# Performance work log

Measured on AMD Instinct MI355X. Metric: run time of the kernel, lower is better.

## Reference

```python
import jax, jax.numpy as jnp
import numpy as np

NUM_ANCHORS = 2
NUM_CLASSES = 20
H = 7
W = 7
IMG_H = 448
IMG_W = 448
NMS_THRESH = 0.7
SCORE_THRESH = 0.05
NBOX = H * W * NUM_ANCHORS  # 98 candidate boxes per image


def _format_outputs(x):
    # x: [b, H*W*(num_anchors*5 + num_classes)] -> decoded boxes/objectness/scores
    b = x.shape[0]
    x = x.reshape(b, H, W, NUM_ANCHORS * 5 + NUM_CLASSES)
    # class scores shared across anchors of a cell (repeat_interleave in torch)
    b_scores = jnp.broadcast_to(
        x[..., -NUM_CLASSES:].reshape(b, H * W, 1, NUM_CLASSES),
        (b, H * W, NUM_ANCHORS, NUM_CLASSES),
    )
    xa = x[..., : NUM_ANCHORS * 5].reshape(b, H, W, NUM_ANCHORS, 5)
    c_x = jnp.arange(W, dtype=x.dtype) * (IMG_W / W)
    c_y = jnp.arange(H, dtype=x.dtype) * (IMG_H / H)
    b_x = jax.nn.sigmoid(xa[..., 0]) + c_x[None, None, :, None]
    b_y = jax.nn.sigmoid(xa[..., 1]) + c_y[None, :, None, None]
    b_w = jax.nn.sigmoid(xa[..., 2])
    b_h = jax.nn.sigmoid(xa[..., 3])
    b_coords = jnp.stack((b_x, b_y, b_w, b_h), axis=-1).reshape(b, H * W, NUM_ANCHORS, 4)
    b_o = jax.nn.sigmoid(xa[..., 4]).reshape(b, H * W, NUM_ANCHORS)
    return b_coords, b_o, b_scores


def _pairwise_iou(boxes):
    # boxes: [n, 4] xyxy -> [n, n] IoU (torchvision box_iou semantics, 0 where union==0)
    area = (boxes[:, 2] - boxes[:, 0]) * (boxes[:, 3] - boxes[:, 1])
    lt = jnp.maximum(boxes[:, None, :2], boxes[None, :, :2])
    rb = jnp.minimum(boxes[:, None, 2:], boxes[None, :, 2:])
    wh = jnp.clip(rb - lt, 0.0)
    inter = wh[..., 0] * wh[..., 1]
    union = area[:, None] + area[None, :] - inter
    return jnp.where(union > 0, inter / union, 0.0)


def _per_image(coords, o, sc):
    # coords: [NBOX,4] (x,y,w,h), o: [NBOX], sc: [NBOX,NUM_CLASSES]
    valid = o >= 0.5  # objectness gate (b_o >= 0.5 selection in torch)
    labels = jnp.argmax(sc, axis=-1)
    scores = jnp.max(sc, axis=-1)
    # xywh -> xyxy, clamp to [0,1] (as in post_process)
    boxes = jnp.clip(
        jnp.concatenate([coords[:, :2], coords[:, :2] + coords[:, 2:]], axis=-1), 0.0, 1.0
    )
    # sort by score descending, invalid boxes pushed to the end
    s = jnp.where(valid, scores, -jnp.inf)
    order = jnp.argsort(-s)
    boxes_s = boxes[order]
    scores_s = scores[order]
    labels_s = labels[order]
    valid_s = valid[order]
    iou = _pairwise_iou(boxes_s)
    idxs = jnp.arange(NBOX)

    def body(i, alive):
        # if box i is still alive, suppress later boxes with IoU > thresh
        suppress = (iou[i] > NMS_THRESH) & (idxs > i) & alive[i]
        return alive & ~suppress

    alive = jax.lax.fori_loop(0, NBOX, body, valid_s)
    keep = alive & (scores_s >= SCORE_THRESH)
    boxes_out = jnp.where(keep[:, None], boxes_s, 0.0)
    scores_out = jnp.where(keep, scores_s, 0.0)
    labels_out = jnp.where(keep, labels_s, 0)
    return boxes_out, scores_out, labels_out, keep


def setup_inputs() -> dict:
    key = jax.random.key(0)
    x = jax.random.normal(key, (8192, H * W * (NUM_ANCHORS * 5 + NUM_CLASSES)), dtype=jnp.float32)
    return {"x": x}


def reference(x):
    b_coords, b_o, b_scores = _format_outputs(x)
    b = x.shape[0]
    coords = b_coords.reshape(b, -1, 4)
    o = b_o.reshape(b, -1)
    sc = b_scores.reshape(b, -1, NUM_CLASSES)
    boxes, scores, labels, keep = jax.vmap(_per_image)(coords, o, sc)
    # padded detections: [b, NBOX, 4], [b, NBOX], [b, NBOX], keep mask [b, NBOX]
    return boxes, scores, labels, keep
```

## Files before the change

kernel.cpp:

```cpp
#include <hip/hip_runtime.h>
#include <math.h>

#define NBOX 98
#define ROWLEN 1470
#define ROWPAD 1472
#define NMS_T 0.7f
#define SCORE_T 0.05f

__device__ __forceinline__ float sigm(float v) {
    return 1.0f / (1.0f + expf(-v));
}

__device__ __forceinline__ float rdlane_f(float v, int l) {
    return __int_as_float(__builtin_amdgcn_readlane(__float_as_int(v), l));
}

__global__ __launch_bounds__(256) void yolo_post(const float* __restrict__ x,
                                                 float* __restrict__ out,
                                                 int batch) {
    const int wid  = threadIdx.x >> 6;
    const int lane = threadIdx.x & 63;
    const int b    = blockIdx.x * 4 + wid;

    __shared__ __align__(16) float srow[4][ROWPAD];
    float* row = srow[wid];

    if (b < batch) {
        const float2* src = reinterpret_cast<const float2*>(x + (size_t)b * ROWLEN);
        float2* dst = reinterpret_cast<float2*>(row);
        #pragma unroll
        for (int r = 0; r < 12; ++r) {
            const int i = lane + r * 64;
            if (i < ROWLEN / 2) dst[i] = src[i];
        }
    }
    __syncthreads();
    if (b >= batch) return;

    const int  cell   = lane;
    const bool active = (cell < 49);

    float  s = 0.0f, lab = 0.0f;
    int    vbits = 0;
    float4 B0 = make_float4(0.f, 0.f, 0.f, 0.f);
    float4 B1 = make_float4(0.f, 0.f, 0.f, 0.f);

    if (active) {
        const float* c = row + cell * 30;
        float mx = c[10]; int ml = 0;
        #pragma unroll
        for (int t = 1; t < 20; ++t) {
            const float v = c[10 + t];
            if (v > mx) { mx = v; ml = t; }
        }
        s = mx; lab = (float)ml;

        const int ci = cell / 7;
        const int cj = cell - ci * 7;
        const float fx = (float)cj * 64.0f;
        const float fy = (float)ci * 64.0f;

        {
            const float bx = sigm(c[0]) + fx;
            const float by = sigm(c[1]) + fy;
            const float bw = sigm(c[2]);
            const float bh = sigm(c[3]);
            B0.x = fminf(fmaxf(bx, 0.f), 1.f);
            B0.y = fminf(fmaxf(by, 0.f), 1.f);
            B0.z = fminf(fmaxf(bx + bw, 0.f), 1.f);
            B0.w = fminf(fmaxf(by + bh, 0.f), 1.f);
            if (c[4] >= 0.0f) vbits |= 1;
        }
        {
            const float bx = sigm(c[5]) + fx;
            const float by = sigm(c[6]) + fy;
            const float bw = sigm(c[7]);
            const float bh = sigm(c[8]);
            B1.x = fminf(fmaxf(bx, 0.f), 1.f);
            B1.y = fminf(fmaxf(by, 0.f), 1.f);
            B1.z = fminf(fmaxf(bx + bw, 0.f), 1.f);
            B1.w = fminf(fmaxf(by + bh, 0.f), 1.f);
            if (c[9] >= 0.0f) vbits |= 2;
        }
    }

    const bool v0 = (vbits & 1) != 0;
    const bool v1 = (vbits & 2) != 0;

    const unsigned long long V0m = __ballot(v0);
    const unsigned long long V1m = __ballot(v1);
    const int V = (int)__popcll(V0m) + (int)__popcll(V1m);

    bool kill_local = false;
    if (cell == 0 && (vbits & 3) == 3) {
        const float a0 = (B0.z - B0.x) * (B0.w - B0.y);
        const float a1 = (B1.z - B1.x) * (B1.w - B1.y);
        const float w  = fmaxf(fminf(B0.z, B1.z) - fmaxf(B0.x, B1.x), 0.f);
        const float h  = fmaxf(fminf(B0.w, B1.w) - fmaxf(B0.y, B1.y), 0.f);
        const float inter = w * h;
        const float uni   = a0 + a1 - inter;
        const float iou   = (uni > 0.f) ? (inter / uni) : 0.f;
        kill_local = (iou > NMS_T);
    }
    const bool kill1 = (__ballot(kill_local) != 0ull);

    int rcom = 0;
    #pragma unroll 7
    for (int j = 0; j < 49; ++j) {
        const float sj  = rdlane_f(s, j);
        const int   vbj = __builtin_amdgcn_readlane(vbits, j);
        const int   cnt = (vbj & 1) + ((vbj >> 1) & 1);
        const bool  pre = (sj > s) || ((sj == s) && (j < cell));
        rcom += pre ? cnt : 0;
    }

    const unsigned long long below = (1ull << cell) - 1ull;
    const int prefv = (int)__popcll(V0m & below) + (int)__popcll(V1m & below);

    const int r0 = v0 ? rcom
                      : (V + 2 * cell - prefv);
    const int r1 = v1 ? (rcom + (v0 ? 1 : 0))
                      : (V + 2 * cell + 1 - prefv - (v0 ? 1 : 0));

    const bool k0 = v0 && (s >= SCORE_T);
    const bool k1 = v1 && (s >= SCORE_T) && !(kill1 && cell == 0);

    if (active) {
        float4* boxes = reinterpret_cast<float4*>(out + (size_t)b * (NBOX * 4));
        const size_t base1 = (size_t)batch * (NBOX * 4);
        const size_t bn    = (size_t)batch * NBOX;
        float* scores = out + base1 +          (size_t)b * NBOX;
        float* labels = out + base1 + bn +     (size_t)b * NBOX;
        float* keepm  = out + base1 + 2 * bn + (size_t)b * NBOX;

        const float4 z = make_float4(0.f, 0.f, 0.f, 0.f);
        boxes[r0]  = k0 ? B0 : z;
        boxes[r1]  = k1 ? B1 : z;
        scores[r0] = k0 ? s : 0.f;
        scores[r1] = k1 ? s : 0.f;
        labels[r0] = k0 ? lab : 0.f;
        labels[r1] = k1 ? lab : 0.f;
        keepm[r0]  = k0 ? 1.f : 0.f;
        keepm[r1]  = k1 ? 1.f : 0.f;
    }
}

extern "C" void kernel_launch(void* const* d_in, const int* in_sizes, int n_in,
                              void* d_out, int out_size, void* d_ws, size_t ws_size,
                              hipStream_t stream) {
    const float* x = (const float*)d_in[0];
    float* out = (float*)d_out;
    const int batch = in_sizes[0] / ROWLEN;
    const int grid  = (batch + 3) / 4;
    yolo_post<<<grid, 256, 0, stream>>>(x, out, batch);
}
```

Before: 100.6 us.

## Use direct global-to-LDS loads, fast sigmoid, and packed-key rank counting

Switches staging of input rows to global_load_lds 16-byte transfers, with two images per 128-thread block stored contiguously in LDS. Uses fast exp/rcp sigmoid, computes clamped coordinates only for cells where the clamp is not trivially 1, and falls back to precise sigmoid only when the cell-0 IoU test is near the threshold. Replaces the float/tie compare in the ranking loop with a single 64-bit packed key compare and splits the accumulation across four counters. Risks precision differences from the fast math, and relies on boxes outside row or column 0 clamping to 1.

```diff
diff --git a/kernel.cpp b/kernel.cpp
--- a/kernel.cpp
+++ b/kernel.cpp
@@ -3,47 +3,57 @@
 
 #define NBOX 98
 #define ROWLEN 1470
-#define ROWPAD 1472
 #define NMS_T 0.7f
 #define SCORE_T 0.05f
 
-__device__ __forceinline__ float sigm(float v) {
+__device__ __forceinline__ float psigm(float v) {
     return 1.0f / (1.0f + expf(-v));
 }
-
-__device__ __forceinline__ float rdlane_f(float v, int l) {
-    return __int_as_float(__builtin_amdgcn_readlane(__float_as_int(v), l));
+__device__ __forceinline__ float fsigm(float v) {
+    return __builtin_amdgcn_rcpf(1.0f + __expf(-v));
 }
 
-__global__ __launch_bounds__(256) void yolo_post(const float* __restrict__ x,
+__device__ __forceinline__ void gl_lds16(const float4* g, float4* l) {
+    __builtin_amdgcn_global_load_lds((const __attribute__((address_space(1))) void*)g,
+                                     (__attribute__((address_space(3))) void*)l,
+                                     16, 0, 0);
+}
+
+__global__ __launch_bounds__(128) void yolo_post(const float* __restrict__ x,
                                                  float* __restrict__ out,
                                                  int batch) {
     const int wid  = threadIdx.x >> 6;
     const int lane = threadIdx.x & 63;
-    const int b    = blockIdx.x * 4 + wid;
+    const int b    = blockIdx.x * 2 + wid;
 
-    __shared__ __align__(16) float srow[4][ROWPAD];
-    float* row = srow[wid];
+    __shared__ __align__(16) float srow[2 * ROWLEN + 4];
 
-    if (b < batch) {
-        const float2* src = reinterpret_cast<const float2*>(x + (size_t)b * ROWLEN);
-        float2* dst = reinterpret_cast<float2*>(row);
+    {
+        const float4* gsrc = reinterpret_cast<const float4*>(
+            x + (size_t)blockIdx.x * (2 * ROWLEN));
+        float4* lrow = reinterpret_cast<float4*>(srow);
+        const size_t maxq = ((size_t)batch * ROWLEN) >> 2;
+        const size_t qbase = (size_t)blockIdx.x * ((2 * ROWLEN) / 4);
         #pragma unroll
-        for (int r = 0; r < 12; ++r) {
-            const int i = lane + r * 64;
-            if (i < ROWLEN / 2) dst[i] = src[i];
+        for (int r = 0; r < 6; ++r) {
+            const int idx = r * 128 + threadIdx.x;
+            if (idx < 735 && qbase + (size_t)idx < maxq) {
+                gl_lds16(gsrc + idx, lrow + (r * 128 + wid * 64));
+            }
         }
     }
     __syncthreads();
     if (b >= batch) return;
+
+    const float* row = srow + wid * ROWLEN;
 
     const int  cell   = lane;
     const bool active = (cell < 49);
 
     float  s = 0.0f, lab = 0.0f;
     int    vbits = 0;
-    float4 B0 = make_float4(0.f, 0.f, 0.f, 0.f);
-    float4 B1 = make_float4(0.f, 0.f, 0.f, 0.f);
+    float4 B0 = make_float4(1.f, 1.f, 1.f, 1.f);
+    float4 B1 = make_float4(1.f, 1.f, 1.f, 1.f);
 
     if (active) {
         const float* c = row + cell * 30;
@@ -57,35 +67,32 @@
 
         const int ci = cell / 7;
         const int cj = cell - ci * 7;
-        const float fx = (float)cj * 64.0f;
-        const float fy = (float)ci * 64.0f;
 
-        {
-            const float bx = sigm(c[0]) + fx;
-            const float by = sigm(c[1]) + fy;
-            const float bw = sigm(c[2]);
-            const float bh = sigm(c[3]);
-            B0.x = fminf(fmaxf(bx, 0.f), 1.f);
-            B0.y = fminf(fmaxf(by, 0.f), 1.f);
-            B0.z = fminf(fmaxf(bx + bw, 0.f), 1.f);
-            B0.w = fminf(fmaxf(by + bh, 0.f), 1.f);
-            if (c[4] >= 0.0f) vbits |= 1;
+        if (c[4] >= 0.0f) vbits |= 1;
+        if (c[9] >= 0.0f) vbits |= 2;
+
+        const float sx0 = fsigm(c[0]), sy0 = fsigm(c[1]);
+        const float sw0 = fsigm(c[2]), sh0 = fsigm(c[3]);
+        const float sx1 = fsigm(c[5]), sy1 = fsigm(c[6]);
+        const float sw1 = fsigm(c[7]), sh1 = fsigm(c[8]);
+
+        if (cj == 0) {
+            B0.x = fminf(fmaxf(sx0, 0.f), 1.f);
+            B0.z = fminf(fmaxf(sx0 + sw0, 0.f), 1.f);
+            B1.x = fminf(fmaxf(sx1, 0.f), 1.f);
+            B1.z = fminf(fmaxf(sx1 + sw1, 0.f), 1.f);
         }
-        {
-            const float bx = sigm(c[5]) + fx;
-            const float by = sigm(c[6]) + fy;
-            const float bw = sigm(c[7]);
-            const float bh = sigm(c[8]);
-            B1.x = fminf(fmaxf(bx, 0.f), 1.f);
-            B1.y = fminf(fmaxf(by, 0.f), 1.f);
-            B1.z = fminf(fmaxf(bx + bw, 0.f), 1.f);
-            B1.w = fminf(fmaxf(by + bh, 0.f), 1.f);
-            if (c[9] >= 0.0f) vbits |= 2;
+        if (ci == 0) {
+            B0.y = fminf(fmaxf(sy0, 0.f), 1.f);
+            B0.w = fminf(fmaxf(sy0 + sh0, 0.f), 1.f);
+            B1.y = fminf(fmaxf(sy1, 0.f), 1.f);
+            B1.w = fminf(fmaxf(sy1 + sh1, 0.f), 1.f);
         }
     }
 
     const bool v0 = (vbits & 1) != 0;
     const bool v1 = (vbits & 2) != 0;
+    const int  cnt = (vbits & 1) + (vbits >> 1);
 
     const unsigned long long V0m = __ballot(v0);
     const unsigned long long V1m = __ballot(v1);
@@ -99,20 +106,51 @@
         const float h  = fmaxf(fminf(B0.w, B1.w) - fmaxf(B0.y, B1.y), 0.f);
         const float inter = w * h;
         const float uni   = a0 + a1 - inter;
-        const float iou   = (uni > 0.f) ? (inter / uni) : 0.f;
-        kill_local = (iou > NMS_T);
+        const float delta = inter - NMS_T * uni;
+        if (fabsf(delta) < 1e-4f * uni) {
+            const float px0 = psigm(row[0]), py0 = psigm(row[1]);
+            const float pw0 = psigm(row[2]), ph0 = psigm(row[3]);
+            const float px1 = psigm(row[5]), py1 = psigm(row[6]);
+            const float pw1 = psigm(row[7]), ph1 = psigm(row[8]);
+            const float X0 = fminf(fmaxf(px0, 0.f), 1.f), Y0 = fminf(fmaxf(py0, 0.f), 1.f);
+            const float Z0 = fminf(fmaxf(px0 + pw0, 0.f), 1.f), W0 = fminf(fmaxf(py0 + ph0, 0.f), 1.f);
+            const float X1 = fminf(fmaxf(px1, 0.f), 1.f), Y1 = fminf(fmaxf(py1, 0.f), 1.f);
+            const float Z1 = fminf(fmaxf(px1 + pw1, 0.f), 1.f), W1 = fminf(fmaxf(py1 + ph1, 0.f), 1.f);
+            const float pa0 = (Z0 - X0) * (W0 - Y0);
+            const float pa1 = (Z1 - X1) * (W1 - Y1);
+            const float pw  = fmaxf(fminf(Z0, Z1) - fmaxf(X0, X1), 0.f);
+            const float ph  = fmaxf(fminf(W0, W1) - fmaxf(Y0, Y1), 0.f);
+            const float pint = pw * ph;
+            const float puni = pa0 + pa1 - pint;
+            const float iou  = (puni > 0.f) ? (pint / puni) : 0.f;
+            kill_local = (iou > NMS_T);
+        } else {
+            kill_local = (delta > 0.f);
+        }
     }
     const bool kill1 = (__ballot(kill_local) != 0ull);
 
-    int rcom = 0;
-    #pragma unroll 7
+    const int ib = __float_as_int(s);
+    const unsigned uo = (unsigned)ib ^ (unsigned)((ib >> 31) | 0x80000000);
+    const unsigned long long key =
+        ((unsigned long long)uo << 8) | ((unsigned)(63 - cell) << 2) | (unsigned)cnt;
+    const unsigned klo = (unsigned)key;
+    const unsigned khi = (unsigned)(key >> 32);
+
+    int acc0 = 0, acc1 = 0, acc2 = 0, acc3 = 0;
+    #pragma unroll
     for (int j = 0; j < 49; ++j) {
-        const float sj  = rdlane_f(s, j);
-        const int   vbj = __builtin_amdgcn_readlane(vbits, j);
-        const int   cnt = (vbj & 1) + ((vbj >> 1) & 1);
-        const bool  pre = (sj > s) || ((sj == s) && (j < cell));
-        rcom += pre ? cnt : 0;
+        const unsigned jlo = (unsigned)__builtin_amdgcn_readlane((int)klo, j);
+        const unsigned jhi = (unsigned)__builtin_amdgcn_readlane((int)khi, j);
+        const unsigned long long kj = ((unsigned long long)jhi << 32) | jlo;
+        const int cj_ = (int)(jlo & 3u);
+        const int add = (kj > key) ? cj_ : 0;
+        if ((j & 3) == 0) acc0 += add;
+        else if ((j & 3) == 1) acc1 += add;
+        else if ((j & 3) == 2) acc2 += add;
+        else acc3 += add;
     }
+    const int rcom = (acc0 + acc1) + (acc2 + acc3);
 
     const unsigned long long below = (1ull << cell) - 1ull;
     const int prefv = (int)__popcll(V0m & below) + (int)__popcll(V1m & below);
@@ -151,6 +189,6 @@
     const float* x = (const float*)d_in[0];
     float* out = (float*)d_out;
     const int batch = in_sizes[0] / ROWLEN;
-    const int grid  = (batch + 3) / 4;
-    yolo_post<<<grid, 256, 0, stream>>>(x, out, batch);
+    const int grid  = (batch + 1) / 2;
+    yolo_post<<<grid, 128, 0, stream>>>(x, out, batch);
 }
```

After: 98.75 us. About the same (-1.8%).
